# Kernel tuning notes

Measured on AMD Instinct MI355X. Metric: run time of the kernel, lower is better.

Reference implementation:

```python
import jax, jax.numpy as jnp
import numpy as np

V, D, H, B, LA, LC = 50000, 300, 256, 32, 256, 256


def setup_inputs():
    key = jax.random.key(0)
    ks = jax.random.split(key, 20)
    u = lambda k, sh, sc: jax.random.uniform(k, sh, jnp.float32, -sc, sc)
    s = 1.0 / float(np.sqrt(H))
    return {
        "anchor_input": jax.random.randint(ks[0], (B, LA), 0, V),
        "anchor_length": jax.random.randint(ks[1], (B,), 1, LA + 1),
        "candidate_input": jax.random.randint(ks[2], (B, LC), 0, V),
        "candidate_length": jax.random.randint(ks[3], (B,), 1, LC + 1),
        "batch_size": B,
        "emb": jax.random.normal(ks[4], (V, D), jnp.float32) * 0.1,
        "W_ih_a": u(ks[5], (3 * H, D), s),
        "W_hh_a": u(ks[6], (3 * H, H), s),
        "b_ih_a": u(ks[7], (3 * H,), s),
        "b_hh_a": u(ks[8], (3 * H,), s),
        "W_ih_c": u(ks[9], (3 * H, D + H), s),
        "W_hh_c": u(ks[10], (3 * H, H), s),
        "b_ih_c": u(ks[11], (3 * H,), s),
        "b_hh_c": u(ks[12], (3 * H,), s),
        "Wq": u(ks[13], (H, H), s),
        "Wk": u(ks[14], (H, H), s),
        "v_att": u(ks[15], (H,), s),
    }


def _gru_step(x, h, W_ih, W_hh, b_ih, b_hh):
    # torch GRUCell convention (gate order r, z, n)
    gi = x @ W_ih.T + b_ih
    gh = h @ W_hh.T + b_hh
    ir, iz, inn = jnp.split(gi, 3, axis=-1)
    hr, hz, hn = jnp.split(gh, 3, axis=-1)
    r = jax.nn.sigmoid(ir + hr)
    z = jax.nn.sigmoid(iz + hz)
    n = jnp.tanh(inn + r * hn)
    return (1.0 - z) * n + z * h


def _forward(anchor_input, anchor_length, candidate_input, candidate_length,
             emb, W_ih_a, W_hh_a, b_ih_a, b_hh_a,
             W_ih_c, W_hh_c, b_ih_c, b_hh_c, Wq, Wk, v_att):
    Bb = anchor_input.shape[0]
    # ---- anchor encoder: GRU with packed-sequence semantics (zero pad outputs, freeze hidden) ----
    ax = emb[anchor_input].transpose(1, 0, 2)  # [LA, B, D]
    ts_a = jnp.arange(ax.shape[0])

    def a_step(h, inp):
        xt, t = inp
        hn = _gru_step(xt, h, W_ih_a, W_hh_a, b_ih_a, b_hh_a)
        valid = (t < anchor_length)[:, None]
        h = jnp.where(valid, hn, h)
        return h, jnp.where(valid, hn, 0.0)

    h0 = jnp.zeros((Bb, H), ax.dtype)
    anchor_hidden, a_outs = jax.lax.scan(a_step, h0, (ax, ts_a))  # a_outs: [LA, B, H]
    anchor_outputs = a_outs.transpose(1, 0, 2)  # [B, LA, H]
    anchor_emb = a_outs.sum(0) / anchor_length.astype(ax.dtype)[:, None]  # meanVector

    # ---- candidate decoder: per-step additive attention + GRU + length-mask blend ----
    keys = anchor_outputs @ Wk  # [B, LA, H], precomputed once
    cx = emb[candidate_input].transpose(1, 0, 2)  # [LC, B, D]
    ts_c = jnp.arange(cx.shape[0])

    def c_step(h, inp):
        xt, t = inp
        q = h @ Wq  # [B, H] query from previous hidden
        scores = jnp.einsum('blh,h->bl', jnp.tanh(keys + q[:, None, :]), v_att)
        attn = jax.nn.softmax(scores, axis=-1)
        context = jnp.einsum('bl,blh->bh', attn, anchor_outputs)
        hn = _gru_step(jnp.concatenate([xt, context], axis=-1), h,
                       W_ih_c, W_hh_c, b_ih_c, b_hh_c)
        mask = (candidate_length < t).astype(h.dtype)[:, None]  # strict '<' is faithful to source
        h = hn * (1.0 - mask) + mask * h
        return h, h * (1.0 - mask)

    _, c_outs = jax.lax.scan(c_step, anchor_hidden, (cx, ts_c))  # [LC, B, H]
    valid_c = (ts_c[:, None] < candidate_length[None, :]).astype(cx.dtype)[:, :, None]
    candidate_emb = (c_outs * valid_c).sum(0) / candidate_length.astype(cx.dtype)[:, None]
    return anchor_emb, candidate_emb


def reference(anchor_input, anchor_length, candidate_input, candidate_length, batch_size,
              emb, W_ih_a, W_hh_a, b_ih_a, b_hh_a,
              W_ih_c, W_hh_c, b_ih_c, b_hh_c, Wq, Wk, v_att):
    return _forward(anchor_input, anchor_length, candidate_input, candidate_length,
                    emb, W_ih_a, W_hh_a, b_ih_a, b_hh_a,
                    W_ih_c, W_hh_c, b_ih_c, b_hh_c, Wq, Wk, v_att)
```

## Files before the change

### kernel.cpp

```cpp
#include <hip/hip_runtime.h>
#include <hip/hip_fp16.h>
#include <math.h>

#define BB 32
#define LAV 256
#define LCV 256
#define DV 300
#define HV 256
#define G3 768

typedef _Float16 f16x2 __attribute__((ext_vector_type(2)));
union F4H8 { float4 f4; f16x2 h2[4]; };
union U2H4 { uint2 u2; f16x2 h2[2]; };

static __device__ __forceinline__ float rcp_(float x) { return __builtin_amdgcn_rcpf(x); }
static __device__ __forceinline__ float sigm(float x) { return rcp_(1.f + __expf(-x)); }
static __device__ __forceinline__ float tanh_(float x) { return 1.f - 2.f * rcp_(1.f + __expf(2.f * x)); }

__global__ void prep_pack(const float* __restrict__ W_ih_a, const float* __restrict__ W_ih_c,
                          const float* __restrict__ W_hh_a, const float* __restrict__ W_hh_c,
                          const float* __restrict__ Wq,
                          float* __restrict__ WT_a, float* __restrict__ WT_cx,
                          __half* __restrict__ WhaRH, __half* __restrict__ WhaSH,
                          __half* __restrict__ WqH, __half* __restrict__ WrzH,
                          __half* __restrict__ WnH, float* __restrict__ WcxCT)
{
    int i = blockIdx.x * 256 + threadIdx.x;
    switch (blockIdx.y) {
    case 0: if (i < 230400) { int k = i / 768, n = i % 768; WT_a[i] = W_ih_a[n * 300 + k]; } break;
    case 1: if (i < 230400) { int k = i / 768, n = i % 768; WT_cx[i] = W_ih_c[n * 556 + k]; } break;
    case 2: if (i < 98304) { int e = i & 1, r = i >> 1, ii = r & 63, j = r >> 6;
            WhaRH[i] = __float2half(W_hh_a[j * 256 + 2 * ii + e]); } break;
    case 3: if (i < 98304) { int e = i & 1, s = (i >> 1) & 1, r = i >> 2, j = r % 768, i2 = r / 768;
            int k = 2 * (64 + 2 * i2 + s) + e;
            WhaSH[i] = __float2half(W_hh_a[j * 256 + k]); } break;
    case 4: if (i < 65536) { int e = i & 1, r2 = i >> 1, m = r2 & 255, k2 = r2 >> 8;
            WqH[i] = __float2half(Wq[(2 * k2 + e) * 256 + m]); } break;
    case 5: if (i < 262144) { int e = i & 1, r2 = i >> 1, j = r2 & 511, kk = r2 >> 9;
            int kh = kk >> 7, k2i = kk & 127, k = kh * 256 + 2 * k2i + e;
            float v = (k < 256) ? W_hh_c[j * 256 + k] : W_ih_c[j * 556 + 300 + (k - 256)];
            WrzH[i] = __float2half(v); } break;
    case 6: if (i < 131072) { int e = i & 1, r2 = i >> 1, j = r2 & 255, gg = r2 >> 8;
            int slot = gg >> 6, k2i = gg & 63, grp = slot >> 1, kh = slot & 1;
            int kl = kh * 128 + 2 * k2i + e;
            float v = grp ? W_ih_c[(512 + j) * 556 + 300 + kl] : W_hh_c[(512 + j) * 256 + kl];
            WnH[i] = __float2half(v); } break;
    case 7: if (i < 196608) { int k = i / 768, j = i % 768;
            WcxCT[i] = W_ih_c[j * 556 + 300 + k]; } break;
    }
}

template <int MODE>
__global__ __launch_bounds__(256) void gemm_tile(
    const float* __restrict__ X, const int* __restrict__ gidx, int ldx,
    const float* __restrict__ Wt, int K, int Nn,
    const float* __restrict__ bias, float* __restrict__ Cout)
{
    __shared__ __align__(16) float As[32][68];
    __shared__ __align__(16) float Bs[32][68];
    __shared__ int toks[64];
    int tid = threadIdx.x;
    int m0 = blockIdx.x * 64, n0 = blockIdx.y * 64;
    if (tid < 64) {
        int m = m0 + tid;
        if (gidx) { int t = m >> 5, b = m & 31; toks[tid] = gidx[b * LAV + t]; }
        else toks[tid] = m;
    }
    __syncthreads();
    float acc[4][4] = {};
    int tx = tid & 15, ty = tid >> 4;
    for (int k0 = 0; k0 < K; k0 += 32) {
        {
            int r = tid >> 2, cc = (tid & 3) * 8;
            const float* src = X + (size_t)toks[r] * ldx + k0 + cc;
            float4 v0 = {0.f,0.f,0.f,0.f}, v1 = {0.f,0.f,0.f,0.f};
            if (k0 + cc + 3 < K) v0 = *(const float4*)src;
            if (k0 + cc + 7 < K) v1 = *(const float4*)(src + 4);
            As[cc+0][r]=v0.x; As[cc+1][r]=v0.y; As[cc+2][r]=v0.z; As[cc+3][r]=v0.w;
            As[cc+4][r]=v1.x; As[cc+5][r]=v1.y; As[cc+6][r]=v1.z; As[cc+7][r]=v1.w;
        }
        {
            int kr = tid >> 4, c4 = (tid & 15) * 4;
            #pragma unroll
            for (int p = 0; p < 2; ++p) {
                float4 v = {0.f,0.f,0.f,0.f};
                int kg = k0 + kr + p * 16;
                if (kg < K) v = *(const float4*)(Wt + (size_t)kg * Nn + n0 + c4);
                *(float4*)&Bs[kr + p * 16][c4] = v;
            }
        }
        __syncthreads();
        #pragma unroll 8
        for (int kk = 0; kk < 32; ++kk) {
            float4 a4 = *(const float4*)&As[kk][ty * 4];
            float4 b4 = *(const float4*)&Bs[kk][tx * 4];
            acc[0][0]=fmaf(a4.x,b4.x,acc[0][0]); acc[0][1]=fmaf(a4.x,b4.y,acc[0][1]);
            acc[0][2]=fmaf(a4.x,b4.z,acc[0][2]); acc[0][3]=fmaf(a4.x,b4.w,acc[0][3]);
            acc[1][0]=fmaf(a4.y,b4.x,acc[1][0]); acc[1][1]=fmaf(a4.y,b4.y,acc[1][1]);
            acc[1][2]=fmaf(a4.y,b4.z,acc[1][2]); acc[1][3]=fmaf(a4.y,b4.w,acc[1][3]);
            acc[2][0]=fmaf(a4.z,b4.x,acc[2][0]); acc[2][1]=fmaf(a4.z,b4.y,acc[2][1]);
            acc[2][2]=fmaf(a4.z,b4.z,acc[2][2]); acc[2][3]=fmaf(a4.z,b4.w,acc[2][3]);
            acc[3][0]=fmaf(a4.w,b4.x,acc[3][0]); acc[3][1]=fmaf(a4.w,b4.y,acc[3][1]);
            acc[3][2]=fmaf(a4.w,b4.z,acc[3][2]); acc[3][3]=fmaf(a4.w,b4.w,acc[3][3]);
        }
        __syncthreads();
    }
    if (MODE == 0) {
        float4 bz = *(const float4*)&bias[n0 + tx * 4];
        #pragma unroll
        for (int i = 0; i < 4; ++i) {
            int m = m0 + ty * 4 + i;
            float4 o = { acc[i][0] + bz.x, acc[i][1] + bz.y, acc[i][2] + bz.z, acc[i][3] + bz.w };
            *(float4*)&Cout[(size_t)m * Nn + n0 + tx * 4] = o;
        }
    } else if (MODE == 1) {
        int b_ = m0 >> 8;
        int l0 = (m0 & 255) + ty * 4;
        f16x2* TH = (f16x2*)Cout;
        #pragma unroll
        for (int j = 0; j < 4; ++j) {
            int h = n0 + tx * 4 + j;
            size_t base = ((size_t)(b_ * 256 + h)) * 128 + (l0 >> 1);
            f16x2 v01 = { (_Float16)tanh_(acc[0][j]), (_Float16)tanh_(acc[1][j]) };
            f16x2 v23 = { (_Float16)tanh_(acc[2][j]), (_Float16)tanh_(acc[3][j]) };
            TH[base] = v01;
            TH[base + 1] = v23;
        }
    } else {
        int l0 = m0 + ty * 4;
        f16x2* P2 = (f16x2*)Cout;
        #pragma unroll
        for (int j = 0; j < 4; ++j) {
            int col = n0 + tx * 4 + j;
            f16x2 v01 = { (_Float16)acc[0][j], (_Float16)acc[1][j] };
            f16x2 v23 = { (_Float16)acc[2][j], (_Float16)acc[3][j] };
            P2[(size_t)(l0 >> 1) * 768 + col] = v01;
            P2[(size_t)((l0 >> 1) + 1) * 768 + col] = v23;
        }
    }
}

__global__ __launch_bounds__(768) void anchor_rnn(
    const float* __restrict__ GI, const int* __restrict__ lens,
    const float* __restrict__ bhh, const __half* __restrict__ WhaRH,
    const __half* __restrict__ WhaSH,
    float* __restrict__ AO, __half* __restrict__ AOH,
    float* __restrict__ hid, float* __restrict__ outp)
{
    __shared__ float gh[768];
    __shared__ __align__(16) float hs[256];
    __shared__ __align__(16) f16x2 hx2[128];
    __shared__ float bhhS[768];
    int bid = blockIdx.x, tid = threadIdx.x;
    int len = lens[bid];

    f16x2 wreg[64];
    {
        const float4* s = (const float4*)WhaRH + (size_t)tid * 16;
        #pragma unroll
        for (int u = 0; u < 16; ++u) {
            F4H8 c; c.f4 = s[u];
            wreg[4*u+0] = c.h2[0]; wreg[4*u+1] = c.h2[1];
            wreg[4*u+2] = c.h2[2]; wreg[4*u+3] = c.h2[3];
        }
    }
    if (tid < 256) hs[tid] = 0.f;
    if (tid < 128) { f16x2 z = {(_Float16)0.f, (_Float16)0.f}; hx2[tid] = z; }
    bhhS[tid] = bhh[tid];
    float sum = 0.f;
    __syncthreads();

    for (int t = 0; t < LAV; ++t) {
        {
            float a0=0.f,a1=0.f,a2=0.f,a3=0.f;
            const float4* xb = (const float4*)hx2;
            #pragma unroll
            for (int u = 0; u < 16; ++u) {
                F4H8 xv; xv.f4 = xb[u];
                a0 = __builtin_amdgcn_fdot2(wreg[4*u+0], xv.h2[0], a0, false);
                a1 = __builtin_amdgcn_fdot2(wreg[4*u+1], xv.h2[1], a1, false);
                a2 = __builtin_amdgcn_fdot2(wreg[4*u+2], xv.h2[2], a2, false);
                a3 = __builtin_amdgcn_fdot2(wreg[4*u+3], xv.h2[3], a3, false);
            }
            const uint2* wsp = (const uint2*)WhaSH + tid;
            float b0=0.f,b1=0.f;
            #pragma unroll
            for (int i2 = 0; i2 < 32; ++i2) {
                U2H4 w; w.u2 = wsp[(size_t)i2 * 768];
                U2H4 xx; xx.u2 = *(const uint2*)&hx2[64 + 2 * i2];
                b0 = __builtin_amdgcn_fdot2(w.h2[0], xx.h2[0], b0, false);
                b1 = __builtin_amdgcn_fdot2(w.h2[1], xx.h2[1], b1, false);
            }
            gh[tid] = ((a0 + a1) + (a2 + a3)) + (b0 + b1) + bhhS[tid];
        }
        __syncthreads();
        if (tid < 256) {
            const float* gi = GI + ((size_t)t * BB + bid) * G3;
            float r = sigm(gi[tid] + gh[tid]);
            float z = sigm(gi[256 + tid] + gh[256 + tid]);
            float n = tanh_(fmaf(r, gh[512 + tid], gi[512 + tid]));
            float hk = hs[tid];
            float hn = (1.f - z) * n + z * hk;
            bool valid = (t < len);
            float hnew = valid ? hn : hk;
            hs[tid] = hnew;
            float ov = valid ? hn : 0.f;
            AO[((size_t)bid * LAV + t) * HV + tid] = ov;
            AOH[((size_t)bid * LAV + t) * HV + tid] = __float2half(ov);
            sum += ov;
            float other = __shfl_xor(hnew, 1, 64);
            if (!(tid & 1)) {
                f16x2 v = { (_Float16)hnew, (_Float16)other };
                hx2[tid >> 1] = v;
            }
        }
        __syncthreads();
    }
    if (tid < 256) {
        outp[bid * HV + tid] = sum / (float)len;
        hid[bid * HV + tid] = hs[tid];
    }
}

__global__ __launch_bounds__(1024) void cand_rnn(
    const float* __restrict__ GI, const int* __restrict__ lens,
    const float* __restrict__ bhh, const __half* __restrict__ WrzH,
    const __half* __restrict__ WnH, const __half* __restrict__ WqH,
    const float* __restrict__ v_att, const __half* __restrict__ P2H,
    const __half* __restrict__ TH, const float* __restrict__ hid,
    float* __restrict__ outp)
{
    __shared__ __align__(16) f16x2 x2[128];
    __shared__ __align__(16) float hs[256];
    __shared__ float tqs[256];
    __shared__ float vls[256];
    __shared__ __align__(4) __half attnH[256];
    __shared__ __align__(16) float redBig[2048];
    __shared__ __align__(16) float redRZh[1024];
    __shared__ __align__(16) float redNh[1024];
    __shared__ __align__(16) float gateC[768];
    __shared__ float bhhS[768];
    __shared__ float wred[8];

    int tid = threadIdx.x;
    int b = blockIdx.x;
    int len = lens[b];

    const f16x2* Wq2  = (const f16x2*)WqH;
    const f16x2* Wrz2 = (const f16x2*)WrzH;
    const f16x2* Wn2  = (const f16x2*)WnH;
    const f16x2* T2   = (const f16x2*)TH + (size_t)b * 256 * 128;
    const f16x2* P2b  = (const f16x2*)P2H + (size_t)b * 128 * 768;

    if (tid < 256) { hs[tid] = hid[b * HV + tid]; vls[tid] = v_att[tid]; }
    if (tid < 768) bhhS[tid] = bhh[tid];
    __syncthreads();
    if (tid < 128) {
        f16x2 v = { (_Float16)hs[2 * tid], (_Float16)hs[2 * tid + 1] };
        x2[tid] = v;
    }
    __syncthreads();

    float csum = 0.f;

    for (int t = 0; t < LCV; ++t) {
        {
            int m = tid & 255, kc = tid >> 8;
            float a0 = 0.f, a1 = 0.f;
            #pragma unroll 8
            for (int i = 0; i < 32; i += 2) {
                int k2 = kc * 32 + i;
                a0 = __builtin_amdgcn_fdot2(Wq2[k2 * 256 + m], x2[k2], a0, false);
                a1 = __builtin_amdgcn_fdot2(Wq2[(k2 + 1) * 256 + m], x2[k2 + 1], a1, false);
            }
            redBig[kc * 256 + m] = a0 + a1;
        }
        {
            int j = tid & 511, kh2 = tid >> 9;
            float a0 = 0.f, a1 = 0.f;
            #pragma unroll 8
            for (int i = 0; i < 64; i += 2) {
                int kk = kh2 * 64 + i;
                a0 = __builtin_amdgcn_fdot2(Wrz2[(size_t)kk * 512 + j], x2[kk], a0, false);
                a1 = __builtin_amdgcn_fdot2(Wrz2[(size_t)(kk + 1) * 512 + j], x2[kk + 1], a1, false);
            }
            redRZh[tid] = a0 + a1;
        }
        {
            int j = tid & 255, q4 = tid >> 8;
            float a0 = 0.f, a1 = 0.f;
            #pragma unroll 8
            for (int i = 0; i < 32; i += 2) {
                int gg = q4 * 32 + i;
                a0 = __builtin_amdgcn_fdot2(Wn2[(size_t)gg * 256 + j], x2[gg], a0, false);
                a1 = __builtin_amdgcn_fdot2(Wn2[(size_t)(gg + 1) * 256 + j], x2[gg + 1], a1, false);
            }
            redNh[tid] = a0 + a1;
        }
        __syncthreads();
        if (tid < 256) {
            float q = redBig[tid] + redBig[256 + tid] + redBig[512 + tid] + redBig[768 + tid];
            tqs[tid] = tanh_(q);
        }
        __syncthreads();
        {
            int l2 = tid & 127, hg = tid >> 7;
            float s0 = 0.f, s1 = 0.f;
            #pragma unroll 8
            for (int i = 0; i < 32; ++i) {
                int h = hg * 32 + i;
                f16x2 Tv = T2[(size_t)h * 128 + l2];
                float tq = tqs[h], vv = vls[h];
                float T0 = (float)Tv.x, T1 = (float)Tv.y;
                float d0 = fmaxf(fmaf(T0, tq, 1.f), 1e-6f);
                float d1 = fmaxf(fmaf(T1, tq, 1.f), 1e-6f);
                s0 = fmaf(vv * (T0 + tq), rcp_(d0), s0);
                s1 = fmaf(vv * (T1 + tq), rcp_(d1), s1);
            }
            redBig[hg * 256 + 2 * l2] = s0;
            redBig[hg * 256 + 2 * l2 + 1] = s1;
        }
        __syncthreads();
        float sv = 0.f;
        if (tid < 256) {
            #pragma unroll
            for (int hg = 0; hg < 8; ++hg) sv += redBig[hg * 256 + tid];
            float m = sv;
            #pragma unroll
            for (int o = 1; o < 64; o <<= 1) m = fmaxf(m, __shfl_xor(m, o, 64));
            if ((tid & 63) == 0) wred[tid >> 6] = m;
        }
        __syncthreads();
        if (tid < 256) {
            float mx = fmaxf(fmaxf(wred[0], wred[1]), fmaxf(wred[2], wred[3]));
            float e = __expf(sv - mx);
            attnH[tid] = __float2half(e);
            float s = e;
            #pragma unroll
            for (int o = 1; o < 64; o <<= 1) s += __shfl_xor(s, o, 64);
            if ((tid & 63) == 0) wred[4 + (tid >> 6)] = s;
        }
        __syncthreads();
        if (tid < 768) {
            const f16x2* at2 = (const f16x2*)attnH;
            float a0 = 0.f, a1 = 0.f;
            #pragma unroll 8
            for (int l2 = 0; l2 < 128; l2 += 2) {
                a0 = __builtin_amdgcn_fdot2(P2b[(size_t)l2 * 768 + tid], at2[l2], a0, false);
                a1 = __builtin_amdgcn_fdot2(P2b[(size_t)(l2 + 1) * 768 + tid], at2[l2 + 1], a1, false);
            }
            gateC[tid] = a0 + a1;
        }
        __syncthreads();
        if (tid < 256) {
            const float* gi = GI + ((size_t)t * BB + b) * G3;
            float rs = rcp_(wred[4] + wred[5] + wred[6] + wred[7]);
            float rr = (redRZh[tid] + redRZh[512 + tid]) + gateC[tid] * rs;
            float zz = (redRZh[256 + tid] + redRZh[768 + tid]) + gateC[256 + tid] * rs;
            float nh = (redNh[tid] + redNh[256 + tid]) + (redNh[512 + tid] + redNh[768 + tid]);
            float nc = gateC[512 + tid] * rs;
            float r = sigm(gi[tid] + rr + bhhS[tid]);
            float z = sigm(gi[256 + tid] + zz + bhhS[256 + tid]);
            float n = tanh_(gi[512 + tid] + nc + r * (nh + bhhS[512 + tid]));
            float hk = hs[tid];
            float hn = (1.f - z) * n + z * hk;
            float hnew = (len < t) ? hk : hn;
            hs[tid] = hnew;
            if (t < len) csum += hnew;
            float other = __shfl_xor(hnew, 1, 64);
            if ((tid & 1) == 0) {
                f16x2 v = { (_Float16)hnew, (_Float16)other };
                x2[tid >> 1] = v;
            }
        }
        __syncthreads();
    }
    if (tid < 256) outp[8192 + b * HV + tid] = csum / (float)len;
}

extern "C" void kernel_launch(void* const* d_in, const int* in_sizes, int n_in,
                              void* d_out, int out_size, void* d_ws, size_t ws_size,
                              hipStream_t stream) {
    const int* anchor_input     = (const int*)d_in[0];
    const int* anchor_length    = (const int*)d_in[1];
    const int* candidate_input  = (const int*)d_in[2];
    const int* candidate_length = (const int*)d_in[3];
    const float* emb    = (const float*)d_in[5];
    const float* W_ih_a = (const float*)d_in[6];
    const float* W_hh_a = (const float*)d_in[7];
    const float* b_ih_a = (const float*)d_in[8];
    const float* b_hh_a = (const float*)d_in[9];
    const float* W_ih_c = (const float*)d_in[10];
    const float* W_hh_c = (const float*)d_in[11];
    const float* b_ih_c = (const float*)d_in[12];
    const float* b_hh_c = (const float*)d_in[13];
    const float* Wq     = (const float*)d_in[14];
    const float* Wk     = (const float*)d_in[15];
    const float* v_att  = (const float*)d_in[16];
    float* out = (float*)d_out;

    float* ws = (float*)d_ws;
    size_t off = 0;
    float* GI_a  = ws + off; off += (size_t)LAV * BB * G3;
    float* GI_c  = ws + off; off += (size_t)LCV * BB * G3;
    float* AO    = ws + off; off += (size_t)BB * LAV * HV;
    float* hid   = ws + off; off += (size_t)BB * HV;
    float* WT_a  = ws + off; off += 300 * 768;
    float* WT_cx = ws + off; off += 300 * 768;
    __half* TH    = (__half*)(ws + off); off += (size_t)BB * HV * LAV / 2;
    __half* AOH   = (__half*)(ws + off); off += (size_t)BB * LAV * HV / 2;
    __half* WhaRH = (__half*)(ws + off); off += 98304 / 2;
    __half* WhaSH = (__half*)(ws + off); off += 98304 / 2;
    __half* WqH   = (__half*)(ws + off); off += 65536 / 2;
    __half* WrzH  = (__half*)(ws + off); off += 262144 / 2;
    __half* WnH   = (__half*)(ws + off); off += 131072 / 2;
    float* WcxCT  = ws + off; off += 256 * 768;
    __half* P2H = (__half*)GI_a;

    prep_pack<<<dim3(1024, 8), 256, 0, stream>>>(W_ih_a, W_ih_c, W_hh_a, W_hh_c, Wq,
                                                 WT_a, WT_cx, WhaRH, WhaSH, WqH, WrzH, WnH, WcxCT);
    gemm_tile<0><<<dim3(128, 12), 256, 0, stream>>>(emb, anchor_input, DV, WT_a, DV, G3, b_ih_a, GI_a);
    gemm_tile<0><<<dim3(128, 12), 256, 0, stream>>>(emb, candidate_input, DV, WT_cx, DV, G3, b_ih_c, GI_c);
    anchor_rnn<<<32, 768, 0, stream>>>(GI_a, anchor_length, b_hh_a, WhaRH, WhaSH, AO, AOH, hid, out);
    gemm_tile<1><<<dim3(128, 4), 256, 0, stream>>>(AO, nullptr, HV, Wk, HV, HV, nullptr, (float*)TH);
    gemm_tile<2><<<dim3(128, 12), 256, 0, stream>>>(AO, nullptr, HV, WcxCT, HV, G3, nullptr, (float*)P2H);
    cand_rnn<<<32, 1024, 0, stream>>>(GI_c, candidate_length, b_hh_c, WrzH, WnH, WqH,
                                      v_att, P2H, TH, hid, out);
}
```

Before: 3.907 ms.

## Fuse recurrent matvecs into disjoint thread ranges and drop a barrier

The Wq, Wrz and Wn hidden matvecs in the candidate GRU step now each run over the full K dimension in disjoint thread ranges (256 for Wq, 512 for Wrz, 256 for Wn), so no split-K partial sums need reducing. The tanh of the query is computed inline, which removes one __syncthreads and its reduction phase per timestep. The GI gate inputs are loaded early, overlapping the global load with the matvec, and the attention score precomputes v*tq so the inner loop uses one fewer multiply. In exchange each thread runs longer serial dot products, and the three branches are imbalanced in K per thread, which could lengthen the critical path.

```diff
diff --git a/kernel.cpp b/kernel.cpp
--- a/kernel.cpp
+++ b/kernel.cpp
@@ -232,12 +232,12 @@
 {
     __shared__ __align__(16) f16x2 x2[128];
     __shared__ __align__(16) float hs[256];
-    __shared__ float tqs[256];
+    __shared__ __align__(16) float2 tqv[256];
     __shared__ float vls[256];
     __shared__ __align__(4) __half attnH[256];
     __shared__ __align__(16) float redBig[2048];
-    __shared__ __align__(16) float redRZh[1024];
-    __shared__ __align__(16) float redNh[1024];
+    __shared__ __align__(16) float redRZh[512];
+    __shared__ __align__(16) float redNh[256];
     __shared__ __align__(16) float gateC[768];
     __shared__ float bhhS[768];
     __shared__ float wred[8];
@@ -264,58 +264,59 @@
     float csum = 0.f;
 
     for (int t = 0; t < LCV; ++t) {
-        {
-            int m = tid & 255, kc = tid >> 8;
-            float a0 = 0.f, a1 = 0.f;
+        float gir = 0.f, giz = 0.f, gin = 0.f;
+        if (tid < 256) {
+            const float* gi = GI + ((size_t)t * BB + b) * G3 + tid;
+            gir = gi[0]; giz = gi[256]; gin = gi[512];
+            int m = tid;
+            float a0 = 0.f, a1 = 0.f, a2 = 0.f, a3 = 0.f;
             #pragma unroll 8
-            for (int i = 0; i < 32; i += 2) {
-                int k2 = kc * 32 + i;
-                a0 = __builtin_amdgcn_fdot2(Wq2[k2 * 256 + m], x2[k2], a0, false);
+            for (int k2 = 0; k2 < 128; k2 += 4) {
+                a0 = __builtin_amdgcn_fdot2(Wq2[(k2 + 0) * 256 + m], x2[k2 + 0], a0, false);
                 a1 = __builtin_amdgcn_fdot2(Wq2[(k2 + 1) * 256 + m], x2[k2 + 1], a1, false);
-            }
-            redBig[kc * 256 + m] = a0 + a1;
-        }
-        {
-            int j = tid & 511, kh2 = tid >> 9;
-            float a0 = 0.f, a1 = 0.f;
+                a2 = __builtin_amdgcn_fdot2(Wq2[(k2 + 2) * 256 + m], x2[k2 + 2], a2, false);
+                a3 = __builtin_amdgcn_fdot2(Wq2[(k2 + 3) * 256 + m], x2[k2 + 3], a3, false);
+            }
+            float tq = tanh_((a0 + a1) + (a2 + a3));
+            tqv[m] = make_float2(tq, vls[m] * tq);
+        } else if (tid < 768) {
+            int j = tid - 256;
+            float a0 = 0.f, a1 = 0.f, a2 = 0.f, a3 = 0.f;
             #pragma unroll 8
-            for (int i = 0; i < 64; i += 2) {
-                int kk = kh2 * 64 + i;
-                a0 = __builtin_amdgcn_fdot2(Wrz2[(size_t)kk * 512 + j], x2[kk], a0, false);
+            for (int kk = 0; kk < 128; kk += 4) {
+                a0 = __builtin_amdgcn_fdot2(Wrz2[(size_t)(kk + 0) * 512 + j], x2[kk + 0], a0, false);
                 a1 = __builtin_amdgcn_fdot2(Wrz2[(size_t)(kk + 1) * 512 + j], x2[kk + 1], a1, false);
-            }
-            redRZh[tid] = a0 + a1;
-        }
-        {
-            int j = tid & 255, q4 = tid >> 8;
-            float a0 = 0.f, a1 = 0.f;
+                a2 = __builtin_amdgcn_fdot2(Wrz2[(size_t)(kk + 2) * 512 + j], x2[kk + 2], a2, false);
+                a3 = __builtin_amdgcn_fdot2(Wrz2[(size_t)(kk + 3) * 512 + j], x2[kk + 3], a3, false);
+            }
+            redRZh[j] = (a0 + a1) + (a2 + a3);
+        } else {
+            int j = tid - 768;
+            float a0 = 0.f, a1 = 0.f, a2 = 0.f, a3 = 0.f;
             #pragma unroll 8
-            for (int i = 0; i < 32; i += 2) {
-                int gg = q4 * 32 + i;
-                a0 = __builtin_amdgcn_fdot2(Wn2[(size_t)gg * 256 + j], x2[gg], a0, false);
+            for (int gg = 0; gg < 128; gg += 4) {
+                a0 = __builtin_amdgcn_fdot2(Wn2[(size_t)(gg + 0) * 256 + j], x2[gg + 0], a0, false);
                 a1 = __builtin_amdgcn_fdot2(Wn2[(size_t)(gg + 1) * 256 + j], x2[gg + 1], a1, false);
-            }
-            redNh[tid] = a0 + a1;
-        }
-        __syncthreads();
-        if (tid < 256) {
-            float q = redBig[tid] + redBig[256 + tid] + redBig[512 + tid] + redBig[768 + tid];
-            tqs[tid] = tanh_(q);
+                a2 = __builtin_amdgcn_fdot2(Wn2[(size_t)(gg + 2) * 256 + j], x2[gg + 2], a2, false);
+                a3 = __builtin_amdgcn_fdot2(Wn2[(size_t)(gg + 3) * 256 + j], x2[gg + 3], a3, false);
+            }
+            redNh[j] = (a0 + a1) + (a2 + a3);
         }
         __syncthreads();
         {
             int l2 = tid & 127, hg = tid >> 7;
+            const f16x2* Tb = T2 + (size_t)(hg * 32) * 128 + l2;
             float s0 = 0.f, s1 = 0.f;
             #pragma unroll 8
             for (int i = 0; i < 32; ++i) {
-                int h = hg * 32 + i;
-                f16x2 Tv = T2[(size_t)h * 128 + l2];
-                float tq = tqs[h], vv = vls[h];
+                f16x2 Tv = Tb[(size_t)i * 128];
+                float2 tv = tqv[hg * 32 + i];
+                float vv = vls[hg * 32 + i];
                 float T0 = (float)Tv.x, T1 = (float)Tv.y;
-                float d0 = fmaxf(fmaf(T0, tq, 1.f), 1e-6f);
-                float d1 = fmaxf(fmaf(T1, tq, 1.f), 1e-6f);
-                s0 = fmaf(vv * (T0 + tq), rcp_(d0), s0);
-                s1 = fmaf(vv * (T1 + tq), rcp_(d1), s1);
+                float d0 = fmaxf(fmaf(T0, tv.x, 1.f), 1e-6f);
+                float d1 = fmaxf(fmaf(T1, tv.x, 1.f), 1e-6f);
+                s0 = fmaf(fmaf(vv, T0, tv.y), rcp_(d0), s0);
+                s1 = fmaf(fmaf(vv, T1, tv.y), rcp_(d1), s1);
             }
             redBig[hg * 256 + 2 * l2] = s0;
             redBig[hg * 256 + 2 * l2 + 1] = s1;
@@ -353,15 +354,14 @@
         }
         __syncthreads();
         if (tid < 256) {
-            const float* gi = GI + ((size_t)t * BB + b) * G3;
             float rs = rcp_(wred[4] + wred[5] + wred[6] + wred[7]);
-            float rr = (redRZh[tid] + redRZh[512 + tid]) + gateC[tid] * rs;
-            float zz = (redRZh[256 + tid] + redRZh[768 + tid]) + gateC[256 + tid] * rs;
-            float nh = (redNh[tid] + redNh[256 + tid]) + (redNh[512 + tid] + redNh[768 + tid]);
+            float rr = redRZh[tid] + gateC[tid] * rs;
+            float zz = redRZh[256 + tid] + gateC[256 + tid] * rs;
+            float nh = redNh[tid];
             float nc = gateC[512 + tid] * rs;
-            float r = sigm(gi[tid] + rr + bhhS[tid]);
-            float z = sigm(gi[256 + tid] + zz + bhhS[256 + tid]);
-            float n = tanh_(gi[512 + tid] + nc + r * (nh + bhhS[512 + tid]));
+            float r = sigm(gir + rr + bhhS[tid]);
+            float z = sigm(giz + zz + bhhS[256 + tid]);
+            float n = tanh_(gin + nc + r * (nh + bhhS[512 + tid]));
             float hk = hs[tid];
             float hn = (1.f - z) * n + z * hk;
             float hnew = (len < t) ? hk : hn;
```

Result: faster. 3.786 ms (-3.1%).
